# Kernel tuning notes

Measured on AMD Instinct MI355X. Metric: run time of the kernel, lower is better.

The kernel has to match this reference:

```python
import jax, jax.numpy as jnp
import numpy as np

N_NODES = 100_000
N_EDGES = 1_600_000
N_RELS = 16
D_IN = 128
D_OUT = 64


def setup_inputs() -> dict:
    key = jax.random.key(0)
    k_feat, k_w, k_src, k_dst, k_et = jax.random.split(key, 5)
    feat = jax.random.normal(k_feat, (N_NODES, D_IN), dtype=jnp.float32)
    weight = jax.random.normal(k_w, (N_RELS, D_IN, D_OUT), dtype=jnp.float32)
    src = jax.random.randint(k_src, (N_EDGES,), 0, N_NODES, dtype=jnp.int32)
    dst = jax.random.randint(k_dst, (N_EDGES,), 0, N_NODES, dtype=jnp.int32)
    etypes = jnp.sort(jax.random.randint(k_et, (N_EDGES,), 0, N_RELS, dtype=jnp.int32))
    return {"feat": feat, "weight": weight, "src": src, "dst": dst, "etypes": etypes}


def reference(feat, weight, src, dst, etypes):
    # RGCN gather-mm: message m_e = feat[src_e] @ W[etype_e]; out_v = sum_{e: dst_e = v} m_e
    # Efficient form: project all nodes with all relation weights (dense GEMM, small R),
    # then gather the (etype, src) slice per edge and segment-sum into destinations.
    proj = jnp.einsum('nd,rde->rne', feat, weight)          # [R, N, d_out]
    msg = proj[etypes, src]                                  # [E, d_out] irregular gather
    out = jax.ops.segment_sum(msg, dst, num_segments=feat.shape[0])  # [N, d_out] scatter-sum
    return out
```

## Files before the change

kernel.cpp:

```cpp
#include <hip/hip_runtime.h>
#include <hip/hip_bf16.h>


#define NTHREADS 256
#define TM 64

typedef __attribute__((ext_vector_type(8))) __bf16 bf16x8;
typedef __attribute__((ext_vector_type(4))) float f32x4;

__global__ void cvt_w_kernel(const float* __restrict__ w,
                             __bf16* __restrict__ o, int total) {
    int idx = blockIdx.x * 256 + threadIdx.x;
    if (idx >= total) return;
    int r = idx >> 13;
    int rem = idx & 8191;
    int k = rem >> 6;
    int n = rem & 63;
    o[(r << 13) + (n << 7) + k] = (__bf16)w[idx];
}

__global__ __launch_bounds__(NTHREADS)
void proj_all_kernel(const float* __restrict__ feat, const __bf16* __restrict__ wtb,
                     int N, int R, __bf16* __restrict__ projb) {
    __shared__ __bf16 Wt[2][64 * 136];

    int t = threadIdx.x;
    int wave = t >> 6, lane = t & 63;
    int q = lane >> 4, m = lane & 15;
    long node0 = (long)blockIdx.x * 128 + wave * 32;

    bf16x8 a[2][4];
    #pragma unroll
    for (int mt = 0; mt < 2; mt++) {
        long nd = node0 + mt * 16 + m;
        if (nd > N - 1) nd = N - 1;
        const float* arow = feat + nd * 128;
        #pragma unroll
        for (int ks = 0; ks < 4; ks++) {
            float4 fa = *(const float4*)(arow + ks * 32 + q * 8);
            float4 fb = *(const float4*)(arow + ks * 32 + q * 8 + 4);
            bf16x8 v;
            v[0] = (__bf16)fa.x; v[1] = (__bf16)fa.y; v[2] = (__bf16)fa.z; v[3] = (__bf16)fa.w;
            v[4] = (__bf16)fb.x; v[5] = (__bf16)fb.y; v[6] = (__bf16)fb.z; v[7] = (__bf16)fb.w;
            a[mt][ks] = v;
        }
    }

    {
        const __bf16* wg = wtb;
        #pragma unroll
        for (int i = 0; i < 4; i++) {
            int c = t + i * 256;
            int n = c >> 4, kc = c & 15;
            *(bf16x8*)(&Wt[0][n * 136 + kc * 8]) = *(const bf16x8*)(wg + n * 128 + kc * 8);
        }
    }
    __syncthreads();

    for (int r = 0; r < R; r++) {
        int cur = r & 1, nxt = cur ^ 1;

        bf16x8 wreg[4];
        bool pf = (r + 1 < R);
        if (pf) {
            const __bf16* wg = wtb + ((size_t)(r + 1) << 13);
            #pragma unroll
            for (int i = 0; i < 4; i++) {
                int c = t + i * 256;
                int n = c >> 4, kc = c & 15;
                wreg[i] = *(const bf16x8*)(wg + n * 128 + kc * 8);
            }
        }

        f32x4 acc[2][4] = {};
        #pragma unroll
        for (int ks = 0; ks < 4; ks++) {
            bf16x8 b0 = *(const bf16x8*)(&Wt[cur][(0 * 16 + m) * 136 + ks * 32 + q * 8]);
            bf16x8 b1 = *(const bf16x8*)(&Wt[cur][(1 * 16 + m) * 136 + ks * 32 + q * 8]);
            bf16x8 b2 = *(const bf16x8*)(&Wt[cur][(2 * 16 + m) * 136 + ks * 32 + q * 8]);
            bf16x8 b3 = *(const bf16x8*)(&Wt[cur][(3 * 16 + m) * 136 + ks * 32 + q * 8]);
            #pragma unroll
            for (int mt = 0; mt < 2; mt++) {
                acc[mt][0] = __builtin_amdgcn_mfma_f32_16x16x32_bf16(a[mt][ks], b0, acc[mt][0], 0, 0, 0);
                acc[mt][1] = __builtin_amdgcn_mfma_f32_16x16x32_bf16(a[mt][ks], b1, acc[mt][1], 0, 0, 0);
                acc[mt][2] = __builtin_amdgcn_mfma_f32_16x16x32_bf16(a[mt][ks], b2, acc[mt][2], 0, 0, 0);
                acc[mt][3] = __builtin_amdgcn_mfma_f32_16x16x32_bf16(a[mt][ks], b3, acc[mt][3], 0, 0, 0);
            }
        }

        #pragma unroll
        for (int mt = 0; mt < 2; mt++) {
            #pragma unroll
            for (int reg = 0; reg < 4; reg++) {
                long nd = node0 + mt * 16 + q * 4 + reg;
                if (nd < N) {
                    union { unsigned long long u; __bf16 h[4]; } pk;
                    pk.h[0] = (__bf16)acc[mt][0][reg];
                    pk.h[1] = (__bf16)acc[mt][1][reg];
                    pk.h[2] = (__bf16)acc[mt][2][reg];
                    pk.h[3] = (__bf16)acc[mt][3][reg];
                    __builtin_nontemporal_store(pk.u,
                        (unsigned long long*)(projb + ((size_t)r * N + nd) * 64 + m * 4));
                }
            }
        }

        if (pf) {
            #pragma unroll
            for (int i = 0; i < 4; i++) {
                int c = t + i * 256;
                int n = c >> 4, kc = c & 15;
                *(bf16x8*)(&Wt[nxt][n * 136 + kc * 8]) = wreg[i];
            }
        }
        __syncthreads();
    }
}

__global__ __launch_bounds__(1024)
void bucket_hist(const int* __restrict__ dst, int E, int* __restrict__ bhist) {
    __shared__ int lh[1024];
    int t = threadIdx.x;
    lh[t] = 0;
    __syncthreads();
    long base = (long)blockIdx.x * 8192;
    #pragma unroll
    for (int i = 0; i < 8; i++) {
        long e = base + t + 1024 * i;
        if (e < E) atomicAdd(&lh[dst[e] >> 7], 1);
    }
    __syncthreads();
    if (lh[t]) atomicAdd(&bhist[t], lh[t]);
}

__global__ __launch_bounds__(1024)
void bucket_scan(const int* __restrict__ bhist, int NB, int N, int E,
                 int* __restrict__ boff, int* __restrict__ bcur,
                 int* __restrict__ dofs) {
    __shared__ int sm[1024];
    int t = threadIdx.x;
    int v = (t < NB) ? bhist[t] : 0;
    sm[t] = v;
    __syncthreads();
    for (int s = 1; s < 1024; s <<= 1) {
        int add = (t >= s) ? sm[t - s] : 0;
        __syncthreads();
        sm[t] += add;
        __syncthreads();
    }
    if (t < NB) { int ex = sm[t] - v; boff[t] = ex; bcur[t] = ex; }
    if (t == 0) { boff[NB] = E; dofs[N] = E; }
}

__global__ __launch_bounds__(1024)
void bucket_scatter(const int* __restrict__ dst, const int* __restrict__ src,
                    const int* __restrict__ etypes, int E, int N, int NB,
                    int* __restrict__ bcur, int* __restrict__ items) {
    __shared__ int lh[1024], lb[1024];
    int t = threadIdx.x;
    lh[t] = 0;
    __syncthreads();
    long base = (long)blockIdx.x * 8192;
    int bs[8], it[8];
    #pragma unroll
    for (int i = 0; i < 8; i++) {
        long e = base + t + 1024 * i;
        if (e < E) {
            int d = dst[e];
            int bkt = d >> 7;
            bs[i] = bkt;
            it[i] = ((d & 127) << 24) | (etypes[e] * N + src[e]);
            atomicAdd(&lh[bkt], 1);
        } else bs[i] = -1;
    }
    __syncthreads();
    for (int bb = t; bb < NB; bb += 1024) {
        int c = lh[bb];
        lb[bb] = c ? atomicAdd(&bcur[bb], c) : 0;
        lh[bb] = 0;
    }
    __syncthreads();
    #pragma unroll
    for (int i = 0; i < 8; i++) {
        if (bs[i] >= 0) {
            int pos = lb[bs[i]] + atomicAdd(&lh[bs[i]], 1);
            items[pos] = it[i];
        }
    }
}

__global__ __launch_bounds__(256)
void refine_kernel(const int* __restrict__ boff, const int* __restrict__ items,
                   int N, int* __restrict__ pidx, int* __restrict__ dofs) {
    __shared__ int h[128], sc[128], cur[128];
    int b = blockIdx.x, t = threadIdx.x;
    int j0 = boff[b], j1 = boff[b + 1];
    if (t < 128) h[t] = 0;
    __syncthreads();
    for (int j = j0 + t; j < j1; j += 256)
        atomicAdd(&h[((unsigned)items[j]) >> 24], 1);
    __syncthreads();
    if (t < 128) sc[t] = h[t];
    __syncthreads();
    for (int s = 1; s < 128; s <<= 1) {
        int add = (t >= s && t < 128) ? sc[t - s] : 0;
        __syncthreads();
        if (t < 128) sc[t] += add;
        __syncthreads();
    }
    if (t < 128) {
        int ex = sc[t] - h[t];
        cur[t] = ex;
        int v = (b << 7) + t;
        if (v < N) dofs[v] = j0 + ex;
    }
    __syncthreads();
    for (int j = j0 + t; j < j1; j += 256) {
        int it = items[j];
        int dl = ((unsigned)it) >> 24;
        int pos = j0 + atomicAdd(&cur[dl], 1);
        pidx[pos] = it & 0xFFFFFF;
    }
}

__global__ __launch_bounds__(256)
void reduce_kernel(const int* __restrict__ dofs, const int* __restrict__ pidx,
                   const __bf16* __restrict__ projb, int N, float* __restrict__ out) {
    int gid = blockIdx.x * 256 + threadIdx.x;
    int w = gid >> 6, lane = gid & 63;
    int nw = (gridDim.x * 256) >> 6;
    int sub = lane >> 3, c8 = lane & 7;
    for (int v = w; v < N; v += nw) {
        int j0 = dofs[v], j1 = dofs[v + 1];
        float acc[8] = {0.f, 0.f, 0.f, 0.f, 0.f, 0.f, 0.f, 0.f};
        for (int j = j0 + sub; j < j1; j += 8) {
            int p = pidx[j];
            bf16x8 val = *(const bf16x8*)(projb + (size_t)p * 64 + c8 * 8);
            #pragma unroll
            for (int i = 0; i < 8; i++) acc[i] += (float)val[i];
        }
        #pragma unroll
        for (int mask = 8; mask <= 32; mask <<= 1) {
            #pragma unroll
            for (int i = 0; i < 8; i++) acc[i] += __shfl_xor(acc[i], mask, 64);
        }
        if (sub == 0) {
            float* orow = out + (size_t)v * 64;
            #pragma unroll
            for (int i = 0; i < 8; i++) {
                int cp = c8 * 8 + i;
                orow[(cp & 3) * 16 + (cp >> 2)] = acc[i];
            }
        }
    }
}

__global__ __launch_bounds__(NTHREADS)
void rgcn_atomic(const float* __restrict__ feat, const float* __restrict__ weight,
                 const int* __restrict__ src, const int* __restrict__ dst,
                 const int* __restrict__ etypes, int E,
                 float* __restrict__ out) {
    __shared__ __bf16 Wt[64 * 136];
    int b = blockIdx.x;
    int e0 = b * TM;
    int t = threadIdx.x;
    int wave = t >> 6, lane = t & 63;
    int q = lane >> 4, m = lane & 15;
    int wbase = e0 + wave * 16;
    int last = e0 + TM - 1; if (last > E - 1) last = E - 1;
    int rmin = etypes[e0];
    int rmax = etypes[last];
    int em = wbase + m;
    bool rowok = em < E;
    int ei = rowok ? em : E - 1;
    int my_et = rowok ? etypes[em] : -1;
    const float* arow = feat + (long)src[ei] * 128;
    bf16x8 a[4];
    #pragma unroll
    for (int ks = 0; ks < 4; ks++) {
        float4 fa = *(const float4*)(arow + ks * 32 + q * 8);
        float4 fb = *(const float4*)(arow + ks * 32 + q * 8 + 4);
        bf16x8 v;
        v[0] = (__bf16)fa.x; v[1] = (__bf16)fa.y;
        v[2] = (__bf16)fa.z; v[3] = (__bf16)fa.w;
        v[4] = (__bf16)fb.x; v[5] = (__bf16)fb.y;
        v[6] = (__bf16)fb.z; v[7] = (__bf16)fb.w;
        a[ks] = v;
    }
    f32x4 acc0 = {0.f, 0.f, 0.f, 0.f};
    f32x4 acc1 = {0.f, 0.f, 0.f, 0.f};
    f32x4 acc2 = {0.f, 0.f, 0.f, 0.f};
    f32x4 acc3 = {0.f, 0.f, 0.f, 0.f};
    for (int r = rmin; r <= rmax; ++r) {
        if (r != rmin) __syncthreads();
        const float* wg = weight + (r << 13);
        for (int p = t; p < 4096; p += NTHREADS) {
            int n = p & 63, kh = p >> 6;
            float w0 = wg[(kh * 2) * 64 + n];
            float w1 = wg[(kh * 2 + 1) * 64 + n];
            union { unsigned u; __bf16 h[2]; } pk;
            pk.h[0] = (__bf16)w0; pk.h[1] = (__bf16)w1;
            *(unsigned*)&Wt[n * 136 + kh * 2] = pk.u;
        }
        __syncthreads();
        bool on = (my_et == r);
        #pragma unroll
        for (int ks = 0; ks < 4; ks++) {
            bf16x8 af = a[ks];
            if (!on) {
                #pragma unroll
                for (int j = 0; j < 8; j++) af[j] = (__bf16)0.f;
            }
            bf16x8 b0 = *(const bf16x8*)(&Wt[(0 * 16 + m) * 136 + ks * 32 + q * 8]);
            bf16x8 b1 = *(const bf16x8*)(&Wt[(1 * 16 + m) * 136 + ks * 32 + q * 8]);
            bf16x8 b2 = *(const bf16x8*)(&Wt[(2 * 16 + m) * 136 + ks * 32 + q * 8]);
            bf16x8 b3 = *(const bf16x8*)(&Wt[(3 * 16 + m) * 136 + ks * 32 + q * 8]);
            acc0 = __builtin_amdgcn_mfma_f32_16x16x32_bf16(af, b0, acc0, 0, 0, 0);
            acc1 = __builtin_amdgcn_mfma_f32_16x16x32_bf16(af, b1, acc1, 0, 0, 0);
            acc2 = __builtin_amdgcn_mfma_f32_16x16x32_bf16(af, b2, acc2, 0, 0, 0);
            acc3 = __builtin_amdgcn_mfma_f32_16x16x32_bf16(af, b3, acc3, 0, 0, 0);
        }
    }
    #pragma unroll
    for (int reg = 0; reg < 4; reg++) {
        int er = wbase + q * 4 + reg;
        if (er < E) {
            float* orow = out + (long)dst[er] * 64;
            unsafeAtomicAdd(orow + 0 * 16 + m, acc0[reg]);
            unsafeAtomicAdd(orow + 1 * 16 + m, acc1[reg]);
            unsafeAtomicAdd(orow + 2 * 16 + m, acc2[reg]);
            unsafeAtomicAdd(orow + 3 * 16 + m, acc3[reg]);
        }
    }
}

extern "C" void kernel_launch(void* const* d_in, const int* in_sizes, int n_in,
                              void* d_out, int out_size, void* d_ws, size_t ws_size,
                              hipStream_t stream) {
    const float* feat   = (const float*)d_in[0];
    const float* weight = (const float*)d_in[1];
    const int*   src    = (const int*)d_in[2];
    const int*   dst    = (const int*)d_in[3];
    const int*   etypes = (const int*)d_in[4];
    float* out = (float*)d_out;

    int nfeat = in_sizes[0];
    int nw    = in_sizes[1];
    int E     = in_sizes[2];
    int N     = nfeat / 128;
    int R     = nw >> 13;
    int NB    = (N + 127) >> 7;

    size_t o = 0;
    auto take = [&](size_t bytes) { size_t r = o; o = (o + bytes + 255) & ~(size_t)255; return r; };
    size_t o_bhist = take((size_t)NB * 4);
    size_t o_boff  = take((size_t)(NB + 1) * 4);
    size_t o_bcur  = take((size_t)NB * 4);
    size_t o_dofs  = take((size_t)(N + 1) * 4);
    size_t o_items = take((size_t)E * 4);
    size_t o_pidx  = take((size_t)E * 4);
    size_t o_wtb   = take((size_t)nw * 2);
    size_t o_projb = take((size_t)R * N * 64 * 2);
    size_t need = o;

    bool fast = (ws_size >= need) && (NB <= 1024) && ((size_t)R * N < (1u << 24));

    if (fast) {
        char* ws = (char*)d_ws;
        int* bhist = (int*)(ws + o_bhist);
        int* boff  = (int*)(ws + o_boff);
        int* bcur  = (int*)(ws + o_bcur);
        int* dofs  = (int*)(ws + o_dofs);
        int* items = (int*)(ws + o_items);
        int* pidx  = (int*)(ws + o_pidx);
        __bf16* wtb   = (__bf16*)(ws + o_wtb);
        __bf16* projb = (__bf16*)(ws + o_projb);

        int cgrid = (int)(((long)E + 8191) / 8192);

        hipMemsetAsync(bhist, 0, (size_t)NB * 4, stream);
        bucket_hist<<<cgrid, 1024, 0, stream>>>(dst, E, bhist);
        bucket_scan<<<1, 1024, 0, stream>>>(bhist, NB, N, E, boff, bcur, dofs);
        bucket_scatter<<<cgrid, 1024, 0, stream>>>(dst, src, etypes, E, N, NB, bcur, items);
        refine_kernel<<<NB, 256, 0, stream>>>(boff, items, N, pidx, dofs);
        cvt_w_kernel<<<(nw + 255) / 256, 256, 0, stream>>>(weight, wtb, nw);

        proj_all_kernel<<<(N + 127) / 128, NTHREADS, 0, stream>>>(feat, wtb, N, R, projb);
        reduce_kernel<<<2048, 256, 0, stream>>>(dofs, pidx, projb, N, out);
    } else {
        hipMemsetAsync(d_out, 0, (size_t)out_size * sizeof(float), stream);
        int mgrid = (E + TM - 1) / TM;
        rgcn_atomic<<<mgrid, NTHREADS, 0, stream>>>(feat, weight, src, dst, etypes, E, out);
    }
}
```

Before: 258.2 us.

## Split projection over relation groups and load weights directly into registers

```diff
diff --git a/kernel.cpp b/kernel.cpp
--- a/kernel.cpp
+++ b/kernel.cpp
@@ -4,6 +4,7 @@
 
 #define NTHREADS 256
 #define TM 64
+#define RPB 4
 
 typedef __attribute__((ext_vector_type(8))) __bf16 bf16x8;
 typedef __attribute__((ext_vector_type(4))) float f32x4;
@@ -22,8 +23,6 @@
 __global__ __launch_bounds__(NTHREADS)
 void proj_all_kernel(const float* __restrict__ feat, const __bf16* __restrict__ wtb,
                      int N, int R, __bf16* __restrict__ projb) {
-    __shared__ __bf16 Wt[2][64 * 136];
-
     int t = threadIdx.x;
     int wave = t >> 6, lane = t & 63;
     int q = lane >> 4, m = lane & 15;
@@ -46,45 +45,30 @@
         }
     }
 
-    {
-        const __bf16* wg = wtb;
-        #pragma unroll
-        for (int i = 0; i < 4; i++) {
-            int c = t + i * 256;
-            int n = c >> 4, kc = c & 15;
-            *(bf16x8*)(&Wt[0][n * 136 + kc * 8]) = *(const bf16x8*)(wg + n * 128 + kc * 8);
-        }
-    }
-    __syncthreads();
-
-    for (int r = 0; r < R; r++) {
-        int cur = r & 1, nxt = cur ^ 1;
-
-        bf16x8 wreg[4];
-        bool pf = (r + 1 < R);
-        if (pf) {
-            const __bf16* wg = wtb + ((size_t)(r + 1) << 13);
-            #pragma unroll
-            for (int i = 0; i < 4; i++) {
-                int c = t + i * 256;
-                int n = c >> 4, kc = c & 15;
-                wreg[i] = *(const bf16x8*)(wg + n * 128 + kc * 8);
+    int r0 = blockIdx.y * RPB;
+    int r1 = r0 + RPB; if (r1 > R) r1 = R;
+
+    for (int r = r0; r < r1; r++) {
+        const __bf16* wg = wtb + ((size_t)r << 13);
+
+        bf16x8 b[4][4];
+        #pragma unroll
+        for (int nt = 0; nt < 4; nt++) {
+            #pragma unroll
+            for (int ks = 0; ks < 4; ks++) {
+                b[nt][ks] = *(const bf16x8*)(wg + ((nt * 16 + m) << 7) + ks * 32 + q * 8);
             }
         }
 
         f32x4 acc[2][4] = {};
         #pragma unroll
         for (int ks = 0; ks < 4; ks++) {
-            bf16x8 b0 = *(const bf16x8*)(&Wt[cur][(0 * 16 + m) * 136 + ks * 32 + q * 8]);
-            bf16x8 b1 = *(const bf16x8*)(&Wt[cur][(1 * 16 + m) * 136 + ks * 32 + q * 8]);
-            bf16x8 b2 = *(const bf16x8*)(&Wt[cur][(2 * 16 + m) * 136 + ks * 32 + q * 8]);
-            bf16x8 b3 = *(const bf16x8*)(&Wt[cur][(3 * 16 + m) * 136 + ks * 32 + q * 8]);
             #pragma unroll
             for (int mt = 0; mt < 2; mt++) {
-                acc[mt][0] = __builtin_amdgcn_mfma_f32_16x16x32_bf16(a[mt][ks], b0, acc[mt][0], 0, 0, 0);
-                acc[mt][1] = __builtin_amdgcn_mfma_f32_16x16x32_bf16(a[mt][ks], b1, acc[mt][1], 0, 0, 0);
-                acc[mt][2] = __builtin_amdgcn_mfma_f32_16x16x32_bf16(a[mt][ks], b2, acc[mt][2], 0, 0, 0);
-                acc[mt][3] = __builtin_amdgcn_mfma_f32_16x16x32_bf16(a[mt][ks], b3, acc[mt][3], 0, 0, 0);
+                acc[mt][0] = __builtin_amdgcn_mfma_f32_16x16x32_bf16(a[mt][ks], b[0][ks], acc[mt][0], 0, 0, 0);
+                acc[mt][1] = __builtin_amdgcn_mfma_f32_16x16x32_bf16(a[mt][ks], b[1][ks], acc[mt][1], 0, 0, 0);
+                acc[mt][2] = __builtin_amdgcn_mfma_f32_16x16x32_bf16(a[mt][ks], b[2][ks], acc[mt][2], 0, 0, 0);
+                acc[mt][3] = __builtin_amdgcn_mfma_f32_16x16x32_bf16(a[mt][ks], b[3][ks], acc[mt][3], 0, 0, 0);
             }
         }
 
@@ -104,16 +88,6 @@
                 }
             }
         }
-
-        if (pf) {
-            #pragma unroll
-            for (int i = 0; i < 4; i++) {
-                int c = t + i * 256;
-                int n = c >> 4, kc = c & 15;
-                *(bf16x8*)(&Wt[nxt][n * 136 + kc * 8]) = wreg[i];
-            }
-        }
-        __syncthreads();
     }
 }
 
@@ -385,7 +359,8 @@
         refine_kernel<<<NB, 256, 0, stream>>>(boff, items, N, pidx, dofs);
         cvt_w_kernel<<<(nw + 255) / 256, 256, 0, stream>>>(weight, wtb, nw);
 
-        proj_all_kernel<<<(N + 127) / 128, NTHREADS, 0, stream>>>(feat, wtb, N, R, projb);
+        dim3 pgrid((N + 127) / 128, (R + RPB - 1) / RPB);
+        proj_all_kernel<<<pgrid, NTHREADS, 0, stream>>>(feat, wtb, N, R, projb);
         reduce_kernel<<<2048, 256, 0, stream>>>(dofs, pidx, projb, N, out);
     } else {
         hipMemsetAsync(d_out, 0, (size_t)out_size * sizeof(float), stream);
```

Result: slower. 332.3 us (+28.7%).
